# Kernel tuning notes

Measured on AMD Instinct MI355X. Metric: run time of the kernel, lower is better.

The kernel has to match this reference:

```python
import jax, jax.numpy as jnp
import numpy as np
import math

L, C, NH = 6, 512, 8
HD = C // NH
FF = 4 * C
B = 16
IH, IW = 16, 64
RH, RW = 16, 16
T = IH * IW + RH * RW  # 1280 tokens


def _ln(x, w, b):
    m = jnp.mean(x, axis=-1, keepdims=True)
    v = jnp.mean((x - m) ** 2, axis=-1, keepdims=True)
    return (x - m) * jax.lax.rsqrt(v + 1e-5) * w + b


def setup_inputs() -> dict:
    key = jax.random.key(0)
    ks = jax.random.split(key, 16)
    s = 0.02  # gpt_linear_layer_init_std
    def w(k, shape):
        return jax.random.normal(k, shape, jnp.float32) * s
    return {
        "image_tensor": jax.random.normal(ks[0], (B, C, IH, IW), jnp.float32),
        "radar_tensor": jax.random.normal(ks[1], (B, C, RH, RW), jnp.float32),
        "pos_emb": w(ks[2], (1, T, C)),
        "ln1_w": jnp.ones((L, C), jnp.float32),
        "ln1_b": jnp.zeros((L, C), jnp.float32),
        "Wq": w(ks[3], (L, C, C)), "bq": jnp.zeros((L, C), jnp.float32),
        "Wk": w(ks[4], (L, C, C)), "bk": jnp.zeros((L, C), jnp.float32),
        "Wv": w(ks[5], (L, C, C)), "bv": jnp.zeros((L, C), jnp.float32),
        "Wo": w(ks[6], (L, C, C)), "bo": jnp.zeros((L, C), jnp.float32),
        "ln2_w": jnp.ones((L, C), jnp.float32),
        "ln2_b": jnp.zeros((L, C), jnp.float32),
        "W1": w(ks[7], (L, C, FF)), "b1": jnp.zeros((L, FF), jnp.float32),
        "W2": w(ks[8], (L, FF, C)), "b2": jnp.zeros((L, C), jnp.float32),
        "lnf_w": jnp.ones((C,), jnp.float32),
        "lnf_b": jnp.zeros((C,), jnp.float32),
    }


def reference(image_tensor, radar_tensor, pos_emb, ln1_w, ln1_b, Wq, bq, Wk, bk,
              Wv, bv, Wo, bo, ln2_w, ln2_b, W1, b1, W2, b2, lnf_w, lnf_b):
    bz = radar_tensor.shape[0]
    # (B,C,H,W) -> (B,H*W,C) tokens, channels become embedding dim
    img = jnp.transpose(image_tensor, (0, 2, 3, 1)).reshape(bz, IH * IW, C)
    rad = jnp.transpose(radar_tensor, (0, 2, 3, 1)).reshape(bz, RH * RW, C)
    x = pos_emb + jnp.concatenate([img, rad], axis=1)  # (B,T,C); dropout p=0
    scale = 1.0 / math.sqrt(HD)
    for i in range(L):
        h = _ln(x, ln1_w[i], ln1_b[i])
        q = (h @ Wq[i] + bq[i]).reshape(bz, T, NH, HD).transpose(0, 2, 1, 3)
        k = (h @ Wk[i] + bk[i]).reshape(bz, T, NH, HD).transpose(0, 2, 1, 3)
        v = (h @ Wv[i] + bv[i]).reshape(bz, T, NH, HD).transpose(0, 2, 1, 3)
        att = jax.nn.softmax(jnp.einsum('bhqd,bhkd->bhqk', q, k) * scale, axis=-1)
        y = jnp.einsum('bhqk,bhkd->bhqd', att, v)
        y = y.transpose(0, 2, 1, 3).reshape(bz, T, C)
        x = x + (y @ Wo[i] + bo[i])
        h2 = _ln(x, ln2_w[i], ln2_b[i])
        x = x + (jax.nn.relu(h2 @ W1[i] + b1[i]) @ W2[i] + b2[i])
    x = _ln(x, lnf_w, lnf_b)
    # torch .view reinterpretation of contiguous (B,T,C) memory as (B,C,h,w)
    img_out = x[:, :IH * IW, :].reshape(bz, C, IH, IW)
    rad_out = x[:, IH * IW:, :].reshape(bz, C, RH, RW)
    return (img_out, rad_out)
```

## Files before the change

kernel.cpp:

```cpp
#include <hip/hip_runtime.h>
#include <stdint.h>

typedef __attribute__((ext_vector_type(8))) short bf16x8;
typedef __attribute__((ext_vector_type(4))) short bf16x4;
typedef __attribute__((ext_vector_type(4))) float fx4;
typedef __attribute__((ext_vector_type(4))) unsigned short ushx4;
typedef unsigned short ush;

#define DEV __device__ __forceinline__

DEV unsigned short f2bf(float f) {
  unsigned u = __float_as_uint(f);
  u += 0x7fffu + ((u >> 16) & 1u);
  return (unsigned short)(u >> 16);
}

DEV float fast_exp2(float x) { return __builtin_amdgcn_exp2f(x); }

DEV void async16(const void* g, void* l) {
  __builtin_amdgcn_global_load_lds(
      (const __attribute__((address_space(1))) unsigned*)g,
      (__attribute__((address_space(3))) unsigned*)l, 16, 0, 0);
}

#define WSTRIDE 3145728

__global__ __launch_bounds__(256) void k_prep_weights(
    const float* __restrict__ Wq, const float* __restrict__ Wk,
    const float* __restrict__ Wv, const float* __restrict__ Wo,
    const float* __restrict__ W1, const float* __restrict__ W2,
    ush* __restrict__ wbf) {
  __shared__ float tile[32][33];
  int bid = blockIdx.x;
  int l = bid / 3072, r = bid % 3072;
  const float* src; ush* dst; int R, Cc, t;
  if (r < 768) {
    int w = r >> 8; t = r & 255; R = 512; Cc = 512;
    src = (w == 0 ? Wq : (w == 1 ? Wk : Wv)) + (size_t)l * 262144;
    dst = wbf + (size_t)l * WSTRIDE + w * 262144;
  } else if (r < 1024) {
    t = r - 768; R = 512; Cc = 512;
    src = Wo + (size_t)l * 262144; dst = wbf + (size_t)l * WSTRIDE + 786432;
  } else if (r < 2048) {
    t = r - 1024; R = 512; Cc = 2048;
    src = W1 + (size_t)l * 1048576; dst = wbf + (size_t)l * WSTRIDE + 1048576;
  } else {
    t = r - 2048; R = 2048; Cc = 512;
    src = W2 + (size_t)l * 1048576; dst = wbf + (size_t)l * WSTRIDE + 2097152;
  }
  int tpr = Cc >> 5;
  int trow = t / tpr, tcol = t % tpr;
  int tx = threadIdx.x & 31, ty = threadIdx.x >> 5;
#pragma unroll
  for (int i = 0; i < 4; i++) {
    int rr = trow * 32 + ty + i * 8, cc = tcol * 32 + tx;
    tile[ty + i * 8][tx] = src[(size_t)rr * Cc + cc];
  }
  __syncthreads();
#pragma unroll
  for (int i = 0; i < 4; i++) {
    int cc = tcol * 32 + ty + i * 8, rr = trow * 32 + tx;
    dst[(size_t)cc * R + rr] = f2bf(tile[tx][ty + i * 8]);
  }
}

__global__ __launch_bounds__(256) void k_pack_bias(
    const float* __restrict__ bq, const float* __restrict__ bk,
    const float* __restrict__ bv, float* __restrict__ dst) {
  int idx = blockIdx.x * 256 + threadIdx.x;
  if (idx >= 6 * 1536) return;
  int l = idx / 1536, r = idx % 1536;
  float v = (r < 512) ? bq[l * 512 + r]
            : (r < 1024) ? bk[l * 512 + r - 512] : bv[l * 512 + r - 1024];
  dst[idx] = v;
}

__global__ __launch_bounds__(256) void k_embed(
    const float* __restrict__ img, const float* __restrict__ rad,
    const float* __restrict__ pos, float* __restrict__ x) {
  __shared__ float tile[32][33];
  int bid = blockIdx.x;
  int b = bid / 640, r2 = bid % 640;
  int tc = r2 / 40, tt = r2 % 40;
  int tx = threadIdx.x & 31, ty = threadIdx.x >> 5;
#pragma unroll
  for (int i = 0; i < 4; i++) {
    int c = tc * 32 + ty + i * 8, t = tt * 32 + tx;
    float v = (t < 1024) ? img[(size_t)(b * 512 + c) * 1024 + t]
                         : rad[(size_t)(b * 512 + c) * 256 + (t - 1024)];
    tile[ty + i * 8][tx] = v;
  }
  __syncthreads();
#pragma unroll
  for (int i = 0; i < 4; i++) {
    int t = tt * 32 + ty + i * 8, c = tc * 32 + tx;
    x[(size_t)(b * 1280 + t) * 512 + c] = tile[tx][ty + i * 8] + pos[(size_t)t * 512 + c];
  }
}

__global__ __launch_bounds__(256) void k_ln_bf16(
    const float* __restrict__ x, const float* __restrict__ w,
    const float* __restrict__ bia, ush* __restrict__ h) {
  int wave = threadIdx.x >> 6, lane = threadIdx.x & 63;
  int row = blockIdx.x * 4 + wave;
  int c0 = lane * 8;
  const float4* xr = (const float4*)(x + (size_t)row * 512 + c0);
  float4 a = xr[0], b4 = xr[1];
  float v[8] = {a.x, a.y, a.z, a.w, b4.x, b4.y, b4.z, b4.w};
  float s = 0.f, s2 = 0.f;
#pragma unroll
  for (int e = 0; e < 8; e++) { s += v[e]; s2 += v[e] * v[e]; }
#pragma unroll
  for (int mask = 1; mask < 64; mask <<= 1) {
    s += __shfl_xor(s, mask, 64);
    s2 += __shfl_xor(s2, mask, 64);
  }
  float mean = s * (1.f / 512.f);
  float var = s2 * (1.f / 512.f) - mean * mean;
  float rstd = rsqrtf(var + 1e-5f);
  bf16x8 o;
#pragma unroll
  for (int e = 0; e < 8; e++)
    o[e] = (short)f2bf((v[e] - mean) * rstd * w[c0 + e] + bia[c0 + e]);
  *(bf16x8*)(h + (size_t)row * 512 + c0) = o;
}

__global__ __launch_bounds__(256) void k_ln_final(
    const float* __restrict__ x, const float* __restrict__ w,
    const float* __restrict__ bia, float* __restrict__ out) {
  int wave = threadIdx.x >> 6, lane = threadIdx.x & 63;
  int row = blockIdx.x * 4 + wave;
  int c0 = lane * 8;
  const float4* xr = (const float4*)(x + (size_t)row * 512 + c0);
  float4 a = xr[0], b4 = xr[1];
  float v[8] = {a.x, a.y, a.z, a.w, b4.x, b4.y, b4.z, b4.w};
  float s = 0.f, s2 = 0.f;
#pragma unroll
  for (int e = 0; e < 8; e++) { s += v[e]; s2 += v[e] * v[e]; }
#pragma unroll
  for (int mask = 1; mask < 64; mask <<= 1) {
    s += __shfl_xor(s, mask, 64);
    s2 += __shfl_xor(s2, mask, 64);
  }
  float mean = s * (1.f / 512.f);
  float var = s2 * (1.f / 512.f) - mean * mean;
  float rstd = rsqrtf(var + 1e-5f);
  int b = row / 1280, t = row % 1280;
  size_t orow = (t < 1024) ? ((size_t)b * 1024 + t)
                           : (16384 + (size_t)b * 256 + (t - 1024));
  float o[8];
#pragma unroll
  for (int e = 0; e < 8; e++)
    o[e] = (v[e] - mean) * rstd * w[c0 + e] + bia[c0 + e];
  float4* op = (float4*)(out + orow * 512 + c0);
  op[0] = make_float4(o[0], o[1], o[2], o[3]);
  op[1] = make_float4(o[4], o[5], o[6], o[7]);
}

template <int MODE>
__global__ __launch_bounds__(256) void k_gemm(
    const ush* __restrict__ A, const ush* __restrict__ Wt,
    const float* __restrict__ bias, void* __restrict__ outv,
    ush* __restrict__ vt2, int M, int N, int K) {
  __shared__ char smem[32768];
  char* As = smem;
  char* Bs = smem + 16384;
  const int tid = threadIdx.x;
  const int m0 = blockIdx.y << 7, n0 = blockIdx.x << 7;
  const int lane = tid & 63, wave = tid >> 6;
  const int quad = lane >> 4, l16 = lane & 15;
  const int m_off = (wave & 1) << 6, n_off = (wave >> 1) << 6;
  fx4 acc[4][4];
#pragma unroll
  for (int a = 0; a < 4; a++)
#pragma unroll
    for (int b = 0; b < 4; b++) acc[a][b] = (fx4){0.f, 0.f, 0.f, 0.f};

  for (int k0 = 0; k0 < K; k0 += 64) {
#pragma unroll
    for (int j = 0; j < 4; j++) {
      int f = (j << 8) + tid;
      int row = f >> 3, cph = f & 7;
      int clog = cph ^ (row & 7);
      async16(A + (size_t)(m0 + row) * K + k0 + (clog << 3), As + (f << 4));
    }
#pragma unroll
    for (int j = 0; j < 4; j++) {
      int f = (j << 8) + tid;
      int row = f >> 3, cph = f & 7;
      int clog = cph ^ (row & 7);
      async16(Wt + (size_t)(n0 + row) * K + k0 + (clog << 3), Bs + (f << 4));
    }
    __syncthreads();
#pragma unroll
    for (int ks = 0; ks < 2; ks++) {
      const int chunk = (ks << 2) + quad;
      bf16x8 af[4], bfr[4];
#pragma unroll
      for (int mb = 0; mb < 4; mb++) {
        int rw = m_off + (mb << 4) + l16;
        af[mb] = *(const bf16x8*)(As + rw * 128 + ((chunk ^ (rw & 7)) << 4));
      }
#pragma unroll
      for (int nb = 0; nb < 4; nb++) {
        int rw = n_off + (nb << 4) + l16;
        bfr[nb] = *(const bf16x8*)(Bs + rw * 128 + ((chunk ^ (rw & 7)) << 4));
      }
#pragma unroll
      for (int mb = 0; mb < 4; mb++)
#pragma unroll
        for (int nb = 0; nb < 4; nb++)
          acc[mb][nb] = __builtin_amdgcn_mfma_f32_16x16x32_bf16(
              af[mb], bfr[nb], acc[mb][nb], 0, 0, 0);
    }
    __syncthreads();
  }
#pragma unroll
  for (int mb = 0; mb < 4; mb++) {
#pragma unroll
    for (int nb = 0; nb < 4; nb++) {
      int col = n0 + n_off + (nb << 4) + l16;
      float bval = bias[col];
      if (MODE == 3 && col >= 1024) {
        int row0 = m0 + m_off + (mb << 4) + (quad << 2);
        int b = row0 / 1280, t = row0 - b * 1280;
        ushx4 pk;
#pragma unroll
        for (int i = 0; i < 4; i++) pk[i] = f2bf(acc[mb][nb][i] + bval);
        *(ushx4*)(vt2 + ((size_t)(b * 512 + col - 1024)) * 1280 + t) = pk;
      } else {
#pragma unroll
        for (int i = 0; i < 4; i++) {
          int row = m0 + m_off + (mb << 4) + (quad << 2) + i;
          float v = acc[mb][nb][i] + bval;
          if (MODE == 1) v = fmaxf(v, 0.f);
          if (MODE == 0 || MODE == 1) {
            ((ush*)outv)[(size_t)row * N + col] = f2bf(v);
          } else if (MODE == 3) {
            ((ush*)outv)[(size_t)row * 1024 + col] = f2bf(v);
          } else {
            float* X = (float*)outv;
            X[(size_t)row * N + col] += v;
          }
        }
      }
    }
  }
}

__global__ __launch_bounds__(256) void k_attn(const ush* __restrict__ qk,
                                              const ush* __restrict__ vt,
                                              ush* __restrict__ y) {
  __shared__ char smem[16384];
  char* Ks = smem;
  char* Vs = smem + 8192;
  int id = blockIdx.x;
  int xcd = id & 7, slot = id >> 3;
  int bh = xcd * 16 + slot / 20;
  int qt = slot % 20;
  int b = bh >> 3, h = bh & 7;
  int tid = threadIdx.x;
  int lane = tid & 63, wave = tid >> 6;
  int quad = lane >> 4, l16 = lane & 15;
  int qbase = qt * 64 + wave * 16;
  const float sc = 0.125f * 1.4426950408889634f;

  const ush* qp = qk + (size_t)(b * 1280 + qbase + l16) * 1024 + h * 64 + quad * 8;
  bf16x8 bq0 = *(const bf16x8*)qp;
  bf16x8 bq1 = *(const bf16x8*)(qp + 32);

  const ush* kbase = qk + (size_t)(b * 1280) * 1024 + 512 + h * 64;
  const ush* vbase = vt + (size_t)(b * 512 + h * 64) * 1280;

  fx4 yacc[4];
#pragma unroll
  for (int nb = 0; nb < 4; nb++) yacc[nb] = (fx4){0.f, 0.f, 0.f, 0.f};
  float lp = 0.f;

  for (int k0 = 0; k0 < 1280; k0 += 64) {
#pragma unroll
    for (int j = 0; j < 2; j++) {
      int f = (j << 8) + tid;
      int key = f >> 3, cph = f & 7, clog = cph ^ (key & 7);
      async16(kbase + (size_t)(k0 + key) * 1024 + (clog << 3), Ks + (f << 4));
    }
#pragma unroll
    for (int j = 0; j < 2; j++) {
      int f = (j << 8) + tid;
      int d = f >> 3, cph = f & 7, clog = cph ^ (d & 7);
      async16(vbase + (size_t)d * 1280 + k0 + (clog << 3), Vs + (f << 4));
    }
    __syncthreads();
#pragma unroll
    for (int g = 0; g < 2; g++) {
      int r0 = g * 32 + l16, r1 = g * 32 + 16 + l16;
      bf16x8 ka0 = *(const bf16x8*)(Ks + r0 * 128 + ((quad ^ (r0 & 7)) << 4));
      bf16x8 ka1 = *(const bf16x8*)(Ks + r0 * 128 + (((4 + quad) ^ (r0 & 7)) << 4));
      bf16x8 kc0 = *(const bf16x8*)(Ks + r1 * 128 + ((quad ^ (r1 & 7)) << 4));
      bf16x8 kc1 = *(const bf16x8*)(Ks + r1 * 128 + (((4 + quad) ^ (r1 & 7)) << 4));
      fx4 s0 = (fx4){0.f, 0.f, 0.f, 0.f}, s1 = (fx4){0.f, 0.f, 0.f, 0.f};
      s0 = __builtin_amdgcn_mfma_f32_16x16x32_bf16(ka0, bq0, s0, 0, 0, 0);
      s0 = __builtin_amdgcn_mfma_f32_16x16x32_bf16(ka1, bq1, s0, 0, 0, 0);
      s1 = __builtin_amdgcn_mfma_f32_16x16x32_bf16(kc0, bq0, s1, 0, 0, 0);
      s1 = __builtin_amdgcn_mfma_f32_16x16x32_bf16(kc1, bq1, s1, 0, 0, 0);
      bf16x8 pf;
      float ls = 0.f;
#pragma unroll
      for (int i = 0; i < 4; i++) {
        float p = fast_exp2(s0[i] * sc);
        ls += p;
        pf[i] = (short)f2bf(p);
      }
#pragma unroll
      for (int i = 0; i < 4; i++) {
        float p = fast_exp2(s1[i] * sc);
        ls += p;
        pf[4 + i] = (short)f2bf(p);
      }
      lp += ls;
#pragma unroll
      for (int nb = 0; nb < 4; nb++) {
        int d = nb * 16 + l16;
        int off0 = g * 64 + (quad << 3);
        int off1 = off0 + 32;
        bf16x4 va = *(const bf16x4*)(Vs + d * 128 +
                                     (((off0 >> 4) ^ (d & 7)) << 4) + (off0 & 15));
        bf16x4 vb = *(const bf16x4*)(Vs + d * 128 +
                                     (((off1 >> 4) ^ (d & 7)) << 4) + (off1 & 15));
        bf16x8 vf = {va[0], va[1], va[2], va[3], vb[0], vb[1], vb[2], vb[3]};
        yacc[nb] = __builtin_amdgcn_mfma_f32_16x16x32_bf16(pf, vf, yacc[nb], 0, 0, 0);
      }
    }
    __syncthreads();
  }
  lp += __shfl_xor(lp, 16, 64);
  lp += __shfl_xor(lp, 32, 64);
  float rl[4];
#pragma unroll
  for (int i = 0; i < 4; i++) rl[i] = 1.0f / __shfl(lp, quad * 4 + i, 16);
#pragma unroll
  for (int nb = 0; nb < 4; nb++)
#pragma unroll
    for (int i = 0; i < 4; i++) {
      int t = qbase + quad * 4 + i;
      int col = h * 64 + nb * 16 + l16;
      y[(size_t)(b * 1280 + t) * 512 + col] = f2bf(yacc[nb][i] * rl[i]);
    }
}

extern "C" void kernel_launch(void* const* d_in, const int* in_sizes, int n_in,
                              void* d_out, int out_size, void* d_ws, size_t ws_size,
                              hipStream_t stream) {
  const float* img = (const float*)d_in[0];
  const float* rad = (const float*)d_in[1];
  const float* pos = (const float*)d_in[2];
  const float* ln1w = (const float*)d_in[3];
  const float* ln1b = (const float*)d_in[4];
  const float* Wq = (const float*)d_in[5];
  const float* bq = (const float*)d_in[6];
  const float* Wk = (const float*)d_in[7];
  const float* bk = (const float*)d_in[8];
  const float* Wv = (const float*)d_in[9];
  const float* bv = (const float*)d_in[10];
  const float* Wo = (const float*)d_in[11];
  const float* bo = (const float*)d_in[12];
  const float* ln2w = (const float*)d_in[13];
  const float* ln2b = (const float*)d_in[14];
  const float* W1 = (const float*)d_in[15];
  const float* b1 = (const float*)d_in[16];
  const float* W2 = (const float*)d_in[17];
  const float* b2 = (const float*)d_in[18];
  const float* lnfw = (const float*)d_in[19];
  const float* lnfb = (const float*)d_in[20];

  char* ws = (char*)d_ws;
  float* xw = (float*)(ws + 0);
  ush* h    = (ush*)(ws + 41943040);
  ush* qk   = (ush*)(ws + 62914560);
  ush* vt   = (ush*)(ws + 104857600);
  ush* y    = (ush*)(ws + 125829120);
  ush* u    = (ush*)(ws + 62914560);
  ush* wbf  = (ush*)(ws + 146800640);
  float* qkvb = (float*)(ws + 184549376);

  k_prep_weights<<<18432, 256, 0, stream>>>(Wq, Wk, Wv, Wo, W1, W2, wbf);
  k_pack_bias<<<36, 256, 0, stream>>>(bq, bk, bv, qkvb);
  k_embed<<<10240, 256, 0, stream>>>(img, rad, pos, xw);

  for (int l = 0; l < 6; l++) {
    const ush* wl = wbf + (size_t)l * WSTRIDE;
    k_ln_bf16<<<5120, 256, 0, stream>>>(xw, ln1w + l * 512, ln1b + l * 512, h);
    k_gemm<3><<<dim3(12, 160), 256, 0, stream>>>(h, wl, qkvb + l * 1536, qk, vt, 20480, 1536, 512);
    k_attn<<<2560, 256, 0, stream>>>(qk, vt, y);
    k_gemm<2><<<dim3(4, 160), 256, 0, stream>>>(y, wl + 786432, bo + l * 512, xw, nullptr, 20480, 512, 512);
    k_ln_bf16<<<5120, 256, 0, stream>>>(xw, ln2w + l * 512, ln2b + l * 512, h);
    k_gemm<1><<<dim3(16, 160), 256, 0, stream>>>(h, wl + 1048576, b1 + l * 2048, u, nullptr, 20480, 2048, 512);
    k_gemm<2><<<dim3(4, 160), 256, 0, stream>>>(u, wl + 2097152, b2 + l * 512, xw, nullptr, 20480, 512, 2048);
  }
  k_ln_final<<<5120, 256, 0, stream>>>(xw, lnfw, lnfb, (float*)d_out);
}
```

Measured before the change: 2.146 ms.

## Fold softmax scale into Q projection and streamline attention inner loop

Pre-multiplies Q by the softmax scale times log2(e) in the QKV GEMM epilogue, so the attention kernel feeds exp2 directly. It also packs probabilities with a hardware bf16 pack instruction and computes row sums with an extra MFMA against a ones vector instead of scalar adds and shuffles. V^T is written in a permuted token order so each lane reads V fragments as one 16-byte LDS load instead of two 8-byte loads. This removes VALU and LDS instructions from the attention loop, at the cost of one more MFMA per step and a tighter coupling between the GEMM layout and the attention kernel.

Result: faster. 2.037 ms (-5.1%).

```diff
diff --git a/kernel.cpp b/kernel.cpp
--- a/kernel.cpp
+++ b/kernel.cpp
@@ -17,11 +17,19 @@
 
 DEV float fast_exp2(float x) { return __builtin_amdgcn_exp2f(x); }
 
+DEV unsigned pk_bf16(float a, float b) {
+  unsigned r;
+  asm("v_cvt_pk_bf16_f32 %0, %1, %2" : "=v"(r) : "v"(a), "v"(b));
+  return r;
+}
+
 DEV void async16(const void* g, void* l) {
   __builtin_amdgcn_global_load_lds(
       (const __attribute__((address_space(1))) unsigned*)g,
       (__attribute__((address_space(3))) unsigned*)l, 16, 0, 0);
 }
+
+#define QSCALE 0.18033688011112042f
 
 #define WSTRIDE 3145728
 
@@ -224,10 +232,13 @@
       if (MODE == 3 && col >= 1024) {
         int row0 = m0 + m_off + (mb << 4) + (quad << 2);
         int b = row0 / 1280, t = row0 - b * 1280;
+        int u0 = t & 31;
+        int p0 = ((u0 >> 2) & 3) * 8 + ((u0 & 16) >> 2);
+        int tp = (t & ~31) + p0;
         ushx4 pk;
 #pragma unroll
         for (int i = 0; i < 4; i++) pk[i] = f2bf(acc[mb][nb][i] + bval);
-        *(ushx4*)(vt2 + ((size_t)(b * 512 + col - 1024)) * 1280 + t) = pk;
+        *(ushx4*)(vt2 + ((size_t)(b * 512 + col - 1024)) * 1280 + tp) = pk;
       } else {
 #pragma unroll
         for (int i = 0; i < 4; i++) {
@@ -237,6 +248,7 @@
           if (MODE == 0 || MODE == 1) {
             ((ush*)outv)[(size_t)row * N + col] = f2bf(v);
           } else if (MODE == 3) {
+            if (col < 512) v *= QSCALE;
             ((ush*)outv)[(size_t)row * 1024 + col] = f2bf(v);
           } else {
             float* X = (float*)outv;
@@ -263,7 +275,6 @@
   int lane = tid & 63, wave = tid >> 6;
   int quad = lane >> 4, l16 = lane & 15;
   int qbase = qt * 64 + wave * 16;
-  const float sc = 0.125f * 1.4426950408889634f;
 
   const ush* qp = qk + (size_t)(b * 1280 + qbase + l16) * 1024 + h * 64 + quad * 8;
   bf16x8 bq0 = *(const bf16x8*)qp;
@@ -272,10 +283,14 @@
   const ush* kbase = qk + (size_t)(b * 1280) * 1024 + 512 + h * 64;
   const ush* vbase = vt + (size_t)(b * 512 + h * 64) * 1280;
 
+  bf16x8 ones;
+#pragma unroll
+  for (int e = 0; e < 8; e++) ones[e] = (short)0x3F80;
+
   fx4 yacc[4];
 #pragma unroll
   for (int nb = 0; nb < 4; nb++) yacc[nb] = (fx4){0.f, 0.f, 0.f, 0.f};
-  float lp = 0.f;
+  fx4 ysum = (fx4){0.f, 0.f, 0.f, 0.f};
 
   for (int k0 = 0; k0 < 1280; k0 += 64) {
 #pragma unroll
@@ -303,41 +318,28 @@
       s0 = __builtin_amdgcn_mfma_f32_16x16x32_bf16(ka1, bq1, s0, 0, 0, 0);
       s1 = __builtin_amdgcn_mfma_f32_16x16x32_bf16(kc0, bq0, s1, 0, 0, 0);
       s1 = __builtin_amdgcn_mfma_f32_16x16x32_bf16(kc1, bq1, s1, 0, 0, 0);
-      bf16x8 pf;
-      float ls = 0.f;
-#pragma unroll
-      for (int i = 0; i < 4; i++) {
-        float p = fast_exp2(s0[i] * sc);
-        ls += p;
-        pf[i] = (short)f2bf(p);
-      }
-#pragma unroll
-      for (int i = 0; i < 4; i++) {
-        float p = fast_exp2(s1[i] * sc);
-        ls += p;
-        pf[4 + i] = (short)f2bf(p);
-      }
-      lp += ls;
+      float p0 = fast_exp2(s0[0]), p1 = fast_exp2(s0[1]);
+      float p2 = fast_exp2(s0[2]), p3 = fast_exp2(s0[3]);
+      float p4 = fast_exp2(s1[0]), p5 = fast_exp2(s1[1]);
+      float p6 = fast_exp2(s1[2]), p7 = fast_exp2(s1[3]);
+      unsigned w0 = pk_bf16(p0, p1), w1 = pk_bf16(p2, p3);
+      unsigned w2 = pk_bf16(p4, p5), w3 = pk_bf16(p6, p7);
+      int4 pi = make_int4((int)w0, (int)w1, (int)w2, (int)w3);
+      bf16x8 pf = *(bf16x8*)&pi;
+      ysum = __builtin_amdgcn_mfma_f32_16x16x32_bf16(pf, ones, ysum, 0, 0, 0);
 #pragma unroll
       for (int nb = 0; nb < 4; nb++) {
         int d = nb * 16 + l16;
-        int off0 = g * 64 + (quad << 3);
-        int off1 = off0 + 32;
-        bf16x4 va = *(const bf16x4*)(Vs + d * 128 +
-                                     (((off0 >> 4) ^ (d & 7)) << 4) + (off0 & 15));
-        bf16x4 vb = *(const bf16x4*)(Vs + d * 128 +
-                                     (((off1 >> 4) ^ (d & 7)) << 4) + (off1 & 15));
-        bf16x8 vf = {va[0], va[1], va[2], va[3], vb[0], vb[1], vb[2], vb[3]};
+        bf16x8 vf = *(const bf16x8*)(Vs + d * 128 +
+                                     (((g * 4 + quad) ^ (d & 7)) << 4));
         yacc[nb] = __builtin_amdgcn_mfma_f32_16x16x32_bf16(pf, vf, yacc[nb], 0, 0, 0);
       }
     }
     __syncthreads();
   }
-  lp += __shfl_xor(lp, 16, 64);
-  lp += __shfl_xor(lp, 32, 64);
   float rl[4];
 #pragma unroll
-  for (int i = 0; i < 4; i++) rl[i] = 1.0f / __shfl(lp, quad * 4 + i, 16);
+  for (int i = 0; i < 4; i++) rl[i] = 1.0f / ysum[i];
 #pragma unroll
   for (int nb = 0; nb < 4; nb++)
 #pragma unroll
```
